# Performance work log

Measured on AMD Instinct MI355X. Metric: run time of the kernel, lower is better.

The kernel has to match this reference:

```python
import jax, jax.numpy as jnp
import numpy as np

T, B, D_IN = 1024, 64, 17
H_MAIN = 150   # per-direction hidden of main bi-GRU (hidden_dim=300)
H_HIER = 128   # per-direction hidden of hier bi-GRU (hier_hidden=256)
M = 16         # uniform measure length (eoM fires every M steps)
N_MEAS = T // M
N_PITCH, N_KS = 35, 15
PAD_P, PAD_K = 34, 14


def _gru(x, Wih, Whh, bih, bhh):
    # x: [T, N, D]; torch GRU gate order is (r, z, n)
    H = Whh.shape[1]
    gi_all = jnp.einsum('tnd,gd->tng', x, Wih) + bih  # input-side gates, precomputed

    def step(h, gi):
        gh = h @ Whh.T + bhh
        ir, iz, inn = jnp.split(gi, 3, axis=-1)
        hr, hz, hn = jnp.split(gh, 3, axis=-1)
        r = jax.nn.sigmoid(ir + hr)
        z = jax.nn.sigmoid(iz + hz)
        n = jnp.tanh(inn + r * hn)
        h_new = (1.0 - z) * n + z * h
        return h_new, h_new

    h0 = jnp.zeros((x.shape[1], H), x.dtype)
    _, ys = jax.lax.scan(step, h0, gi_all)
    return ys


def _bigru(x, pf, pb):
    yf = _gru(x, *pf)
    yb = _gru(x[::-1], *pb)[::-1]
    return jnp.concatenate([yf, yb], axis=-1)


def _ce(logits, targets, pad_idx):
    # mean cross-entropy with ignore_index=pad_idx
    logp = jax.nn.log_softmax(logits, axis=-1)
    mask = (targets != pad_idx).astype(logits.dtype)
    nll = -jnp.take_along_axis(logp, targets[:, None], axis=1)[:, 0]
    return jnp.sum(nll * mask) / jnp.maximum(jnp.sum(mask), 1.0)


def _forward(sentences, mWih_f, mWhh_f, mbih_f, mbhh_f, mWih_b, mWhh_b, mbih_b, mbhh_b,
             hWih_f, hWhh_f, hbih_f, hbhh_f, hWih_b, hWhh_b, hbih_b, hbhh_b,
             Wq, bq, Wv, bv, Wp, bp, Wk, bk, pitches, keysignatures):
    # main bi-GRU over full sequences: [T, B, 300]
    rnn_out = _bigru(sentences, (mWih_f, mWhh_f, mbih_f, mbhh_f),
                     (mWih_b, mWhh_b, mbih_b, mbhh_b))
    H2 = rnn_out.shape[-1]
    # carve uniform measures: [T,B,H2] -> [M, B*N_MEAS, H2]
    seg = rnn_out.reshape(N_MEAS, M, B, H2).transpose(1, 2, 0, 3).reshape(M, B * N_MEAS, H2)
    hier = _bigru(seg, (hWih_f, hWhh_f, hbih_f, hbhh_f),
                  (hWih_b, hWhh_b, hbih_b, hbhh_b))  # [M, B*N_MEAS, 256]
    HH = hier.shape[-1]
    # attention per measure: query = value = hier outputs [B*N_MEAS, M, 256]
    hv = hier.reshape(M, B, N_MEAS, HH).transpose(1, 2, 0, 3).reshape(B * N_MEAS, M, HH)
    q = hv @ Wq.T + bq
    v = hv @ Wv.T + bv
    attn = jax.nn.softmax(jnp.einsum('nld,nmd->nlm', q, v), axis=-1)
    ctx = jnp.einsum('nlm,nmd->nd', attn, hv).reshape(B, N_MEAS, HH)  # sum over l of attn@value
    # repeat each measure context over its M timesteps: [T, B, 256]
    ctx_t = jnp.repeat(ctx, M, axis=1).transpose(1, 0, 2)
    stacked = jnp.concatenate([rnn_out, ctx_t], axis=-1)  # [T, B, 556]
    out_pitch = stacked @ Wp.T + bp   # [T, B, 35]
    out_ks = ctx_t @ Wk.T + bk        # [T, B, 15]
    return (_ce(out_pitch.reshape(-1, N_PITCH), pitches.reshape(-1), PAD_P)
            + _ce(out_ks.reshape(-1, N_KS), keysignatures.reshape(-1), PAD_K))


def setup_inputs() -> dict:
    key = jax.random.key(0)
    ks = jax.random.split(key, 32)

    def w(i, *shape):
        return jax.random.normal(ks[i], shape, jnp.float32) * 0.05

    G_M, G_H = 3 * H_MAIN, 3 * H_HIER
    inp = {
        'sentences': jax.random.normal(ks[0], (T, B, D_IN), jnp.float32),
        'pitches': jax.random.randint(ks[1], (T, B), 0, PAD_P),
        'keysignatures': jax.random.randint(ks[2], (T, B), 0, PAD_K),
        'sentences_len': jnp.full((B,), T, dtype=jnp.int32),
        'eoM': jnp.tile(((jnp.arange(T) % M) == M - 1).astype(jnp.int32)[:, None], (1, B)),
        'mWih_f': w(3, G_M, D_IN), 'mWhh_f': w(4, G_M, H_MAIN), 'mbih_f': w(5, G_M), 'mbhh_f': w(6, G_M),
        'mWih_b': w(7, G_M, D_IN), 'mWhh_b': w(8, G_M, H_MAIN), 'mbih_b': w(9, G_M), 'mbhh_b': w(10, G_M),
        'hWih_f': w(11, G_H, 2 * H_MAIN), 'hWhh_f': w(12, G_H, H_HIER), 'hbih_f': w(13, G_H), 'hbhh_f': w(14, G_H),
        'hWih_b': w(15, G_H, 2 * H_MAIN), 'hWhh_b': w(16, G_H, H_HIER), 'hbih_b': w(17, G_H), 'hbhh_b': w(18, G_H),
        'Wq': w(19, 2 * H_HIER, 2 * H_HIER), 'bq': w(20, 2 * H_HIER),
        'Wv': w(21, 2 * H_HIER, 2 * H_HIER), 'bv': w(22, 2 * H_HIER),
        'Wp': w(23, N_PITCH, 2 * H_MAIN + 2 * H_HIER), 'bp': w(24, N_PITCH),
        'Wk': w(25, N_KS, 2 * H_HIER), 'bk': w(26, N_KS),
    }
    return inp


def reference(sentences, pitches, keysignatures, sentences_len, eoM,
              mWih_f, mWhh_f, mbih_f, mbhh_f, mWih_b, mWhh_b, mbih_b, mbhh_b,
              hWih_f, hWhh_f, hbih_f, hbhh_f, hWih_b, hWhh_b, hbih_b, hbhh_b,
              Wq, bq, Wv, bv, Wp, bp, Wk, bk):
    # sentences_len/eoM encode the (uniform) measure structure M=16, full lengths;
    # the segment layout is baked in statically, so they are structural constants here.
    return _forward(sentences, mWih_f, mWhh_f, mbih_f, mbhh_f, mWih_b, mWhh_b, mbih_b, mbhh_b,
                    hWih_f, hWhh_f, hbih_f, hbhh_f, hWih_b, hWhh_b, hbih_b, hbhh_b,
                    Wq, bq, Wv, bv, Wp, bp, Wk, bk, pitches, keysignatures)
```

## Files before the change

kernel.cpp:

```cpp
#include <hip/hip_runtime.h>
#include <cstddef>

constexpr int kT   = 1024;
constexpr int kB   = 64;
constexpr int kDIN = 17;
constexpr int kHM  = 150;
constexpr int kHH  = 128;
constexpr int kM   = 16;
constexpr int kD2  = 300;
constexpr int kNP  = 35;
constexpr int kNK  = 15;

constexpr size_t OFF_RNN16  = 0;
constexpr size_t OFF_HV16   = 10485760;
constexpr size_t OFF_PTPACK = 19988480;
constexpr size_t OFF_U      = 20021248;
constexpr size_t OFF_W      = 20021504;
constexpr size_t OFF_C0     = 20021760;
constexpr size_t OFF_ACC    = 20021776;
constexpr size_t OFF_KSLOGP = 20021792;
constexpr size_t OFF_CLOG   = 20083232;
constexpr size_t OFF_BPACK  = 20318752;
constexpr size_t OFF_BPACKL = 20490784;

typedef __bf16 bf16x8 __attribute__((ext_vector_type(8)));
typedef float f32x4 __attribute__((ext_vector_type(4)));

__device__ __forceinline__ unsigned short f2bf(float f) {
  unsigned u = __float_as_uint(f);
  u += 0x7FFFu + ((u >> 16) & 1u);
  return (unsigned short)(u >> 16);
}
__device__ __forceinline__ float bf2f(unsigned short v) {
  return __uint_as_float(((unsigned)v) << 16);
}
__device__ __forceinline__ float sigm(float x) {
  return __builtin_amdgcn_rcpf(1.f + __expf(-x));
}
__device__ __forceinline__ float tanh_fast(float x) {
  return 1.f - 2.f * __builtin_amdgcn_rcpf(__expf(2.f * x) + 1.f);
}

__global__ __launch_bounds__(640, 2) void k_mega(
    const float* __restrict__ x,
    const float* __restrict__ mWih_f, const float* __restrict__ mWhh_f,
    const float* __restrict__ mWih_b, const float* __restrict__ mWhh_b,
    const float* __restrict__ mbih_f, const float* __restrict__ mbhh_f,
    const float* __restrict__ mbih_b, const float* __restrict__ mbhh_b,
    const float* __restrict__ hWih_f, const float* __restrict__ hWhh_f,
    const float* __restrict__ hWih_b, const float* __restrict__ hWhh_b,
    const float* __restrict__ Wp,
    const float* __restrict__ Wq, const float* __restrict__ bq,
    const float* __restrict__ Wv, const float* __restrict__ bv,
    unsigned short* __restrict__ rnn16,
    unsigned short* __restrict__ bpack,
    unsigned short* __restrict__ bpackL,
    unsigned short* __restrict__ pp,
    float* __restrict__ u, float* __restrict__ w,
    float* __restrict__ c0, float* __restrict__ acc)
{
  __shared__ __align__(16) unsigned short hx[2][160];
  __shared__ __align__(16) unsigned short hist[2][16][160];
  __shared__ __align__(16) unsigned short xall[kT][32];
  const int blk = blockIdx.x;
  if (blk < 128) {
    const int d = blk & 1, b = blk >> 1;
    const int tid = threadIdx.x, wv = tid >> 6, lane = tid & 63;
    const int col = lane & 15, q8 = (lane >> 4) * 8;
    for (int i = tid; i < 2 * 160; i += 640) ((unsigned short*)hx)[i] = 0;
    for (int i = tid; i < 2 * 16 * 160; i += 640) ((unsigned short*)hist)[i] = 0;
    for (int i = tid; i < kT * 32; i += 640) {
      const int t = i >> 5, c = i & 31;
      xall[t][c] = (c < kDIN) ? f2bf(x[((size_t)t * kB + b) * kDIN + c]) : (unsigned short)0;
    }
    const float* bih = d ? mbih_b : mbih_f;
    const float* bhh = d ? mbhh_b : mbhh_f;
    const float* Wihd = d ? mWih_b : mWih_f;
    const float* Whhd = d ? mWhh_b : mWhh_f;
    const int j = wv * 16 + col;
    const bool actv = (lane < 16) && (j < kHM);
    float br = 0.f, bz = 0.f, bnx = 0.f, bnh = 0.f;
    if (actv) {
      br  = bih[j] + bhh[j];
      bz  = bih[150 + j] + bhh[150 + j];
      bnx = bih[300 + j];
      bnh = bhh[300 + j];
    }
    bf16x8 bw[3][6];
    const int gts[3] = { wv, 10 + wv, 20 + wv };
#pragma unroll
    for (int gi = 0; gi < 3; gi++) {
      const int slot = gts[gi] * 16 + col;
      const int type = slot / 160, jh = slot - type * 160;
      const int row = type * 150 + jh;
      const bool valid = (jh < 150);
#pragma unroll
      for (int kt = 0; kt < 6; kt++) {
        union { bf16x8 v; unsigned short us[8]; } tmp;
#pragma unroll
        for (int jj = 0; jj < 8; jj++) {
          float f = 0.f;
          if (valid) {
            if (kt < 5) {
              const int k = kt * 32 + (lane >> 4) * 8 + jj;
              if (k < 150) f = Whhd[row * 150 + k];
            } else {
              const int k = (lane >> 4) * 8 + jj;
              if (k < 17) f = Wihd[row * 17 + k];
            }
          }
          tmp.us[jj] = f2bf(f);
        }
        bw[gi][kt] = tmp.v;
      }
    }
    float h_old = 0.f;
    __syncthreads();

    for (int t = 0; t < kT; t++) {
      const int tx = d ? (kT - 1 - t) : t;
      const int buf = t & 1;
      bf16x8 afr[6];
#pragma unroll
      for (int kt = 0; kt < 5; kt++) afr[kt] = *(const bf16x8*)&hx[buf][kt * 32 + q8];
      afr[5] = *(const bf16x8*)&xall[tx][q8];
      f32x4 aR0 = (f32x4)(0.f), aR1 = (f32x4)(0.f);
      f32x4 aZ0 = (f32x4)(0.f), aZ1 = (f32x4)(0.f);
      f32x4 aN0 = (f32x4)(0.f), aN1 = (f32x4)(0.f);
      f32x4 aX  = (f32x4)(0.f);
#pragma unroll
      for (int kt = 0; kt < 6; kt++) {
        const bf16x8 af = afr[kt];
        if ((kt & 1) == 0) {
          aR0 = __builtin_amdgcn_mfma_f32_16x16x32_bf16(af, bw[0][kt], aR0, 0, 0, 0);
          aZ0 = __builtin_amdgcn_mfma_f32_16x16x32_bf16(af, bw[1][kt], aZ0, 0, 0, 0);
          aN0 = __builtin_amdgcn_mfma_f32_16x16x32_bf16(af, bw[2][kt], aN0, 0, 0, 0);
        } else if (kt < 5) {
          aR1 = __builtin_amdgcn_mfma_f32_16x16x32_bf16(af, bw[0][kt], aR1, 0, 0, 0);
          aZ1 = __builtin_amdgcn_mfma_f32_16x16x32_bf16(af, bw[1][kt], aZ1, 0, 0, 0);
          aN1 = __builtin_amdgcn_mfma_f32_16x16x32_bf16(af, bw[2][kt], aN1, 0, 0, 0);
        } else {
          aR1 = __builtin_amdgcn_mfma_f32_16x16x32_bf16(af, bw[0][5], aR1, 0, 0, 0);
          aZ1 = __builtin_amdgcn_mfma_f32_16x16x32_bf16(af, bw[1][5], aZ1, 0, 0, 0);
          aX  = __builtin_amdgcn_mfma_f32_16x16x32_bf16(af, bw[2][5], aX, 0, 0, 0);
        }
      }
      if (actv) {
        const float r = sigm(aR0[0] + aR1[0] + br);
        const float z = sigm(aZ0[0] + aZ1[0] + bz);
        const float n = tanh_fast(aX[0] + bnx + r * (aN0[0] + aN1[0] + bnh));
        h_old = (1.f - z) * n + z * h_old;
        const unsigned short us = f2bf(h_old);
        hx[buf ^ 1][j] = us;
        hist[(t >> 4) & 1][t & 15][j] = us;
      }
      __syncthreads();
      if ((t & 15) == 15) {
        const int hb = (t >> 4) & 1;
        const int toff = tid / 40, ch = tid - toff * 40;
        const int tg = t - 15 + toff;
        const int txg = d ? (kT - 1 - tg) : tg;
        *(ushort4*)&rnn16[((size_t)txg * kB + b) * 320 + d * 160 + ch * 4] =
            *(const ushort4*)&hist[hb][toff][ch * 4];
      }
    }
  } else if (blk < 199) {
    const int sub = threadIdx.x >> 6, lane = threadIdx.x & 63;
    int bid = (blk - 128) * 10 + sub;
    if (bid >= 702) return;
    if (bid < 672) {
      const int kt = bid % 14;
      const int nt = (bid / 14) % 24;
      const int d  = bid / (14 * 24);
      const float* Wih = d ? hWih_b : hWih_f;
      const float* Whh = d ? hWhh_b : hWhh_f;
      const int n = nt * 16 + (lane & 15);
      const int kbase = kt * 32 + (lane >> 4) * 8;
      unsigned short* dst = bpack + ((((size_t)d * 24 + nt) * 14 + kt) * 64 + lane) * 8;
#pragma unroll
      for (int jj = 0; jj < 8; jj++) {
        const int k = kbase + jj;
        float f = 0.f;
        if (kt < 10) {
          if (k < 150) f = Wih[n * 300 + k];
          else if (k >= 160 && k < 310) f = Wih[n * 300 + (k - 10)];
        } else {
          f = Whh[n * 128 + (k - 320)];
        }
        dst[jj] = f2bf(f);
      }
    } else {
      bid -= 672;
      const int kt = bid % 10, nt = bid / 10;
      const int n = nt * 16 + (lane & 15);
      const int kbase = kt * 32 + (lane >> 4) * 8;
      unsigned short* dst = bpackL + (((size_t)bid) * 64 + lane) * 8;
#pragma unroll
      for (int jj = 0; jj < 8; jj++) {
        const int k = kbase + jj;
        float f = 0.f;
        if (n < kNP) {
          if (k < 150) f = Wp[n * 556 + k];
          else if (k >= 160 && k < 310) f = Wp[n * 556 + (k - 10)];
        }
        dst[jj] = f2bf(f);
      }
    }
  } else if (blk < 212) {
    const int sub = threadIdx.x >> 6, lane = threadIdx.x & 63;
    const int bid = (blk - 199) * 10 + sub;
    if (bid >= 128) return;
    const int kt = bid & 7, nt = bid >> 3;
    const int c = nt * 16 + (lane & 15);
    const int e0 = kt * 32 + (lane >> 4) * 8;
    float av[8];
#pragma unroll
    for (int jj = 0; jj < 8; jj++) av[jj] = 0.f;
    for (int a = 0; a < 256; a++) {
      const float wq = Wq[a * 256 + c];
#pragma unroll
      for (int jj = 0; jj < 8; jj++) av[jj] += wq * Wv[a * 256 + e0 + jj];
    }
    unsigned short* dst = pp + ((size_t)bid * 64 + lane) * 8;
#pragma unroll
    for (int jj = 0; jj < 8; jj++) dst[jj] = f2bf(av[jj]);
  } else {
    const int a = threadIdx.x;
    if (a >= 256) return;
    float us = 0.f, ws = 0.f;
    for (int jj = 0; jj < 256; jj++) {
      us += Wq[jj * 256 + a] * bv[jj];
      ws += bq[jj] * Wv[jj * 256 + a];
    }
    u[a] = us; w[a] = ws;
    if (a == 0) {
      float cc = 0.f;
      for (int jj = 0; jj < 256; jj++) cc += bq[jj] * bv[jj];
      c0[0] = cc;
      acc[0] = acc[1] = acc[2] = acc[3] = 0.f;
    }
  }
}

__global__ __launch_bounds__(512, 1) void k_hier_mfma(
    const unsigned short* __restrict__ rnn16,
    const unsigned short* __restrict__ bpack,
    const float* __restrict__ bihf, const float* __restrict__ bhhf,
    const float* __restrict__ bihb, const float* __restrict__ bhhb,
    unsigned short* __restrict__ hv16)
{
  const int d = blockIdx.x & 1;
  const int bn0 = (blockIdx.x >> 1) * 16;
  const int tid = threadIdx.x;
  const int w = tid >> 6;
  const int lane = tid & 63;
  const int q = lane >> 4, col = lane & 15, q8 = q * 8;

  __shared__ __align__(16) unsigned short x_s[2][16][328];
  __shared__ __align__(16) unsigned short h_s[16][136];

  for (int i = tid; i < 16 * 136; i += 512) ((unsigned short*)h_s)[i] = 0;
  const float* bih = d ? bihb : bihf;
  const float* bhh = d ? bhhb : bhhf;
  const int j = w * 16 + col;
  const float biR  = bih[j] + bhh[j];
  const float biZ  = bih[128 + j] + bhh[128 + j];
  const float biNX = bih[256 + j];
  const float biNH = bhh[256 + j];
  float h32r[4] = {0.f, 0.f, 0.f, 0.f};

  bf16x8 bw[3][14];
  const unsigned short* bpd = bpack + (size_t)d * 24 * 14 * 64 * 8;
  const int nts[3] = { w, 8 + w, 16 + w };
#pragma unroll
  for (int gi = 0; gi < 3; gi++)
#pragma unroll
    for (int kt = 0; kt < 14; kt++)
      bw[gi][kt] = *(const bf16x8*)&bpd[(((size_t)nts[gi] * 14 + kt) * 64 + lane) * 8];

  {
    const int mx0 = d ? 15 : 0;
    for (int i = tid; i < 640; i += 512) {
      const int r = i / 40, c = i - r * 40;
      const int bn = bn0 + r, bb = bn >> 6, nn = bn & 63;
      *(uint4*)&x_s[0][r][c * 8] =
          *(const uint4*)&rnn16[((size_t)(nn * 16 + mx0) * 64 + bb) * 320 + c * 8];
    }
  }
  __syncthreads();

  for (int m = 0; m < kM; m++) {
    const int mx = d ? (15 - m) : m;
    const int buf = m & 1;
    f32x4 aR = (f32x4)(0.f), aZ = (f32x4)(0.f), aNX = (f32x4)(0.f), aNH = (f32x4)(0.f);
#pragma unroll
    for (int kt = 0; kt < 14; kt++) {
      const bf16x8 af = (kt < 10) ? *(const bf16x8*)&x_s[buf][col][kt * 32 + q8]
                                  : *(const bf16x8*)&h_s[col][(kt - 10) * 32 + q8];
      aR = __builtin_amdgcn_mfma_f32_16x16x32_bf16(af, bw[0][kt], aR, 0, 0, 0);
      aZ = __builtin_amdgcn_mfma_f32_16x16x32_bf16(af, bw[1][kt], aZ, 0, 0, 0);
      if (kt < 10) aNX = __builtin_amdgcn_mfma_f32_16x16x32_bf16(af, bw[2][kt], aNX, 0, 0, 0);
      else         aNH = __builtin_amdgcn_mfma_f32_16x16x32_bf16(af, bw[2][kt], aNH, 0, 0, 0);
    }
    __syncthreads();
#pragma unroll
    for (int i = 0; i < 4; i++) {
      const int row = q * 4 + i;
      const float rr = sigm(aR[i] + biR);
      const float zz = sigm(aZ[i] + biZ);
      const float nn2 = tanh_fast(aNX[i] + biNX + rr * (aNH[i] + biNH));
      const float hnew = (1.f - zz) * nn2 + zz * h32r[i];
      h32r[i] = hnew;
      const unsigned short us = f2bf(hnew);
      h_s[row][j] = us;
      hv16[((size_t)(bn0 + row) * kM + mx) * 256 + d * kHH + j] = us;
    }
    if (m + 1 < kM) {
      const int mxn = d ? (15 - (m + 1)) : (m + 1);
      for (int i = tid; i < 640; i += 512) {
        const int r = i / 40, c = i - r * 40;
        const int bn = bn0 + r, bb = bn >> 6, nn = bn & 63;
        *(uint4*)&x_s[buf ^ 1][r][c * 8] =
            *(const uint4*)&rnn16[((size_t)(nn * 16 + mxn) * 64 + bb) * 320 + c * 8];
      }
    }
    __syncthreads();
  }
}

__global__ __launch_bounds__(256) void k_attn_ctx(
    const unsigned short* __restrict__ hv16, const unsigned short* __restrict__ ptpack,
    const float* __restrict__ u, const float* __restrict__ w,
    const float* __restrict__ c0p,
    const float* __restrict__ Wp, const float* __restrict__ bp,
    const float* __restrict__ Wk, const float* __restrict__ bk,
    float* __restrict__ clog, float* __restrict__ kslogp) {
  const int tid = threadIdx.x;
  const int wv = tid >> 6, lane = tid & 63, col = lane & 15, q = lane >> 4, q8 = q * 8;
  __shared__ __align__(16) unsigned short hv16s[16][264];
  __shared__ __align__(16) unsigned short Ts16[16][264];
  __shared__ __align__(16) float W2[50][260];
  __shared__ __align__(16) float cs[256];
  __shared__ float pu[16][17], pw[16][17];
  __shared__ float uh[16], wh[16], SM[16];
  __shared__ float As[16][17];
  __shared__ float arr[64];
  __shared__ float bps[35], bks[15];
  const float c0 = c0p[0];
  for (int i = tid; i < 35 * 256; i += 256) { const int r = i >> 8, c = i & 255; W2[r][c] = Wp[r * 556 + 300 + c]; }
  for (int i = tid; i < 15 * 256; i += 256) { const int r = i >> 8, c = i & 255; W2[35 + r][c] = Wk[r * 256 + c]; }
  if (tid < 35) bps[tid] = bp[tid];
  else if (tid < 50) bks[tid - 35] = bk[tid - 35];
  bf16x8 bpt[4][8];
#pragma unroll
  for (int i2 = 0; i2 < 4; i2++)
#pragma unroll
    for (int kt = 0; kt < 8; kt++)
      bpt[i2][kt] = *(const bf16x8*)&ptpack[((((size_t)(wv * 4 + i2)) * 8 + kt) * 64 + lane) * 8];

  for (int ni = 0; ni < 16; ni++) {
    const int n = blockIdx.x * 16 + ni;
    {
      const unsigned short* src = hv16 + (size_t)n * 4096;
      const int row = tid >> 4, ci = (tid & 15) * 16;
#pragma unroll
      for (int k = 0; k < 16; k += 4)
        *(ushort4*)&hv16s[row][ci + k] = *(const ushort4*)&src[row * 256 + ci + k];
    }
    __syncthreads();
    {
      f32x4 acc4[4];
#pragma unroll
      for (int i2 = 0; i2 < 4; i2++) acc4[i2] = (f32x4)(0.f);
#pragma unroll
      for (int kt = 0; kt < 8; kt++) {
        const bf16x8 af = *(const bf16x8*)&hv16s[col][kt * 32 + q8];
#pragma unroll
        for (int i2 = 0; i2 < 4; i2++)
          acc4[i2] = __builtin_amdgcn_mfma_f32_16x16x32_bf16(af, bpt[i2][kt], acc4[i2], 0, 0, 0);
      }
#pragma unroll
      for (int i2 = 0; i2 < 4; i2++) {
        const int nt = wv * 4 + i2;
#pragma unroll
        for (int i = 0; i < 4; i++) Ts16[q * 4 + i][nt * 16 + col] = f2bf(acc4[i2][i]);
      }
    }
    {
      const int l = tid >> 4, s = tid & 15;
      float su = 0.f, sw = 0.f;
#pragma unroll
      for (int a0 = 0; a0 < 16; a0++) {
        const int a = s * 16 + a0;
        const float hvv = bf2f(hv16s[l][a]);
        su += hvv * u[a];
        sw += hvv * w[a];
      }
      pu[l][s] = su; pw[l][s] = sw;
    }
    __syncthreads();
    if (tid < 16) { float s2 = 0.f; for (int s = 0; s < 16; s++) s2 += pu[tid][s]; uh[tid] = s2; }
    else if (tid < 32) { float s2 = 0.f; for (int s = 0; s < 16; s++) s2 += pw[tid - 16][s]; wh[tid - 16] = s2; }
    __syncthreads();
    if (tid < 64) {
      f32x4 sa = (f32x4)(0.f);
#pragma unroll
      for (int kt = 0; kt < 8; kt++) {
        const bf16x8 af  = *(const bf16x8*)&hv16s[col][kt * 32 + q8];
        const bf16x8 bts = *(const bf16x8*)&Ts16[col][kt * 32 + q8];
        sa = __builtin_amdgcn_mfma_f32_16x16x32_bf16(af, bts, sa, 0, 0, 0);
      }
#pragma unroll
      for (int i = 0; i < 4; i++) {
        const int l = q * 4 + i;
        float sc = sa[i] + c0 + uh[l] + wh[col];
        float mxv = sc;
#pragma unroll
        for (int o = 8; o >= 1; o >>= 1) mxv = fmaxf(mxv, __shfl_xor(mxv, o, 16));
        const float e = __expf(sc - mxv);
        float se = e;
#pragma unroll
        for (int o = 8; o >= 1; o >>= 1) se += __shfl_xor(se, o, 16);
        As[l][col] = e / se;
      }
    }
    __syncthreads();
    if (tid < 16) {
      float s = 0.f;
      for (int l2 = 0; l2 < 16; l2++) s += As[l2][tid];
      SM[tid] = s;
    }
    __syncthreads();
    {
      float cv = 0.f;
#pragma unroll
      for (int m2 = 0; m2 < 16; m2++) cv += SM[m2] * bf2f(hv16s[m2][tid]);
      cs[tid] = cv;
    }
    __syncthreads();
    {
      const int o = tid >> 2, s = tid & 3;
      float v = 0.f;
      if (o < 50) {
        for (int k0 = 0; k0 < 64; k0 += 4) {
          const int k = s * 64 + k0;
          const float4 wq = *(const float4*)&W2[o][k];
          const float4 cq = *(const float4*)&cs[k];
          v += wq.x * cq.x + wq.y * cq.y + wq.z * cq.z + wq.w * cq.w;
        }
      }
      v += __shfl_xor(v, 1);
      v += __shfl_xor(v, 2);
      if (o < 50 && s == 0) arr[o] = v;
    }
    __syncthreads();
    if (tid < 35) clog[n * kNP + tid] = arr[tid] + bps[tid];
    if (tid >= 64 && tid < 80) {
      const int t2 = tid - 64;
      float kk = (t2 < 15) ? arr[35 + t2] + bks[t2] : -1e30f;
      float mxv = kk;
#pragma unroll
      for (int off = 8; off >= 1; off >>= 1) mxv = fmaxf(mxv, __shfl_xor(mxv, off, 16));
      const float e = (t2 < 15) ? __expf(kk - mxv) : 0.f;
      float se = e;
#pragma unroll
      for (int off = 8; off >= 1; off >>= 1) se += __shfl_xor(se, off, 16);
      if (t2 < 15) kslogp[n * kNK + t2] = kk - mxv - __logf(se);
    }
    __syncthreads();
  }
}

__global__ __launch_bounds__(256, 2) void k_loss_mfma(
    const unsigned short* __restrict__ rnn16,
    const unsigned short* __restrict__ bpackL,
    const float* __restrict__ clog,
    const float* __restrict__ ks_logp,
    const int* __restrict__ pitches, const int* __restrict__ kss,
    float* __restrict__ acc) {
  const int tid = threadIdx.x, w = tid >> 6, lane = tid & 63;
  const int col = lane & 15, q = lane >> 4, q8 = q * 8;
  bf16x8 bl[3][10];
#pragma unroll
  for (int nt = 0; nt < 3; nt++)
#pragma unroll
    for (int kt = 0; kt < 10; kt++)
      bl[nt][kt] = *(const bf16x8*)&bpackL[(((size_t)nt * 10 + kt) * 64 + lane) * 8];

  float sp = 0.f, cp = 0.f, sk = 0.f, ck = 0.f;
#pragma unroll
  for (int mt = 0; mt < 2; mt++) {
    const int rowbase = blockIdx.x * 128 + w * 32 + mt * 16;
    f32x4 a0 = (f32x4)(0.f), a1 = (f32x4)(0.f), a2 = (f32x4)(0.f);
#pragma unroll
    for (int kt = 0; kt < 10; kt++) {
      const bf16x8 af = *(const bf16x8*)&rnn16[(size_t)(rowbase + col) * 320 + kt * 32 + q8];
      a0 = __builtin_amdgcn_mfma_f32_16x16x32_bf16(af, bl[0][kt], a0, 0, 0, 0);
      a1 = __builtin_amdgcn_mfma_f32_16x16x32_bf16(af, bl[1][kt], a1, 0, 0, 0);
      a2 = __builtin_amdgcn_mfma_f32_16x16x32_bf16(af, bl[2][kt], a2, 0, 0, 0);
    }
#pragma unroll
    for (int i = 0; i < 4; i++) {
      const int row = rowbase + q * 4 + i;
      const int t = row >> 6, b = row & 63;
      const int bn = b * 64 + (t >> 4);
      const float lg0 = a0[i] + clog[bn * kNP + col];
      const float lg1 = a1[i] + clog[bn * kNP + 16 + col];
      const float lg2 = (col < 3) ? (a2[i] + clog[bn * kNP + 32 + col]) : -1e30f;
      float mx = fmaxf(fmaxf(lg0, lg1), lg2);
#pragma unroll
      for (int o = 8; o >= 1; o >>= 1) mx = fmaxf(mx, __shfl_xor(mx, o, 16));
      float se = __expf(lg0 - mx) + __expf(lg1 - mx) + __expf(lg2 - mx);
#pragma unroll
      for (int o = 8; o >= 1; o >>= 1) se += __shfl_xor(se, o, 16);
      const int tp = pitches[row];
      const float cand = (tp < 16) ? a0[i] : (tp < 32) ? a1[i] : a2[i];
      const float tva = __shfl(cand, (lane & 48) | (tp & 15), 64);
      if (col == 0 && tp != 34) {
        sp += (mx + __logf(se)) - (tva + clog[bn * kNP + tp]);
        cp += 1.f;
      }
      if (col == 1) {
        const int tk = kss[row];
        if (tk != 14) { sk -= ks_logp[bn * kNK + tk]; ck += 1.f; }
      }
    }
  }
#pragma unroll
  for (int o = 32; o >= 1; o >>= 1) {
    sp += __shfl_xor(sp, o, 64);
    cp += __shfl_xor(cp, o, 64);
    sk += __shfl_xor(sk, o, 64);
    ck += __shfl_xor(ck, o, 64);
  }
  if (lane == 0) {
    atomicAdd(&acc[0], sp); atomicAdd(&acc[1], cp);
    atomicAdd(&acc[2], sk); atomicAdd(&acc[3], ck);
  }
}

__global__ void k_final(const float* __restrict__ acc, float* __restrict__ out) {
  out[0] = acc[0] / fmaxf(acc[1], 1.f) + acc[2] / fmaxf(acc[3], 1.f);
}

extern "C" void kernel_launch(void* const* d_in, const int* in_sizes, int n_in,
                              void* d_out, int out_size, void* d_ws, size_t ws_size,
                              hipStream_t stream) {
  (void)in_sizes; (void)n_in; (void)out_size; (void)ws_size;
  const float* sent    = (const float*)d_in[0];
  const int*   pitches = (const int*)d_in[1];
  const int*   kss     = (const int*)d_in[2];
  const float* mWih_f  = (const float*)d_in[5];
  const float* mWhh_f  = (const float*)d_in[6];
  const float* mbih_f  = (const float*)d_in[7];
  const float* mbhh_f  = (const float*)d_in[8];
  const float* mWih_b  = (const float*)d_in[9];
  const float* mWhh_b  = (const float*)d_in[10];
  const float* mbih_b  = (const float*)d_in[11];
  const float* mbhh_b  = (const float*)d_in[12];
  const float* hWih_f  = (const float*)d_in[13];
  const float* hWhh_f  = (const float*)d_in[14];
  const float* hbih_f  = (const float*)d_in[15];
  const float* hbhh_f  = (const float*)d_in[16];
  const float* hWih_b  = (const float*)d_in[17];
  const float* hWhh_b  = (const float*)d_in[18];
  const float* hbih_b  = (const float*)d_in[19];
  const float* hbhh_b  = (const float*)d_in[20];
  const float* Wq      = (const float*)d_in[21];
  const float* bq      = (const float*)d_in[22];
  const float* Wv      = (const float*)d_in[23];
  const float* bv      = (const float*)d_in[24];
  const float* Wp      = (const float*)d_in[25];
  const float* bp      = (const float*)d_in[26];
  const float* Wk      = (const float*)d_in[27];
  const float* bk      = (const float*)d_in[28];
  float* ws  = (float*)d_ws;
  float* out = (float*)d_out;
  unsigned short* rnn16  = (unsigned short*)(ws + OFF_RNN16);
  unsigned short* hv16   = (unsigned short*)(ws + OFF_HV16);
  unsigned short* ptpack = (unsigned short*)(ws + OFF_PTPACK);
  unsigned short* bpackL = (unsigned short*)(ws + OFF_BPACKL);
  unsigned short* bpack  = (unsigned short*)(ws + OFF_BPACK);

  k_mega<<<213, 640, 0, stream>>>(sent,
                                  mWih_f, mWhh_f, mWih_b, mWhh_b,
                                  mbih_f, mbhh_f, mbih_b, mbhh_b,
                                  hWih_f, hWhh_f, hWih_b, hWhh_b, Wp,
                                  Wq, bq, Wv, bv,
                                  rnn16, bpack, bpackL, ptpack,
                                  ws + OFF_U, ws + OFF_W, ws + OFF_C0, ws + OFF_ACC);
  k_hier_mfma<<<512, 512, 0, stream>>>(rnn16, bpack,
                                       hbih_f, hbhh_f, hbih_b, hbhh_b, hv16);
  k_attn_ctx<<<256, 256, 0, stream>>>(hv16, ptpack, ws + OFF_U, ws + OFF_W,
                                      ws + OFF_C0, Wp, bp, Wk, bk,
                                      ws + OFF_CLOG, ws + OFF_KSLOGP);
  k_loss_mfma<<<512, 256, 0, stream>>>(rnn16, bpackL, ws + OFF_CLOG, ws + OFF_KSLOGP,
                                       pitches, kss, ws + OFF_ACC);
  k_final<<<1, 1, 0, stream>>>(ws + OFF_ACC, out);
}
```

Measured before the change: 1.042 ms.

## Prefetch next measure in attention kernel, double grid, fuse final reduction

The attention-context kernel now processes 8 measures per block across 512 blocks instead of 16 across 256. It register-prefetches the next measure's hier outputs while computing the current one, and caches u/w vectors in shared memory. The separate one-thread final kernel is removed: the last loss block, detected by an atomic counter, computes the output. This trims a launch and hides global load latency, at the cost of more per-block setup (W2 loads, ptpack register loads) being repeated twice as often.

```diff
diff --git a/kernel.cpp b/kernel.cpp
--- a/kernel.cpp
+++ b/kernel.cpp
@@ -237,7 +237,7 @@
       float cc = 0.f;
       for (int jj = 0; jj < 256; jj++) cc += bq[jj] * bv[jj];
       c0[0] = cc;
-      acc[0] = acc[1] = acc[2] = acc[3] = 0.f;
+      acc[0] = acc[1] = acc[2] = acc[3] = acc[4] = 0.f;
     }
   }
 }
@@ -341,6 +341,7 @@
   __shared__ __align__(16) unsigned short Ts16[16][264];
   __shared__ __align__(16) float W2[50][260];
   __shared__ __align__(16) float cs[256];
+  __shared__ __align__(16) float us[256], wss[256];
   __shared__ float pu[16][17], pw[16][17];
   __shared__ float uh[16], wh[16], SM[16];
   __shared__ float As[16][17];
@@ -349,6 +350,8 @@
   const float c0 = c0p[0];
   for (int i = tid; i < 35 * 256; i += 256) { const int r = i >> 8, c = i & 255; W2[r][c] = Wp[r * 556 + 300 + c]; }
   for (int i = tid; i < 15 * 256; i += 256) { const int r = i >> 8, c = i & 255; W2[35 + r][c] = Wk[r * 256 + c]; }
+  us[tid] = u[tid];
+  wss[tid] = w[tid];
   if (tid < 35) bps[tid] = bp[tid];
   else if (tid < 50) bks[tid - 35] = bk[tid - 35];
   bf16x8 bpt[4][8];
@@ -358,16 +361,23 @@
     for (int kt = 0; kt < 8; kt++)
       bpt[i2][kt] = *(const bf16x8*)&ptpack[((((size_t)(wv * 4 + i2)) * 8 + kt) * 64 + lane) * 8];
 
-  for (int ni = 0; ni < 16; ni++) {
-    const int n = blockIdx.x * 16 + ni;
-    {
-      const unsigned short* src = hv16 + (size_t)n * 4096;
-      const int row = tid >> 4, ci = (tid & 15) * 16;
-#pragma unroll
-      for (int k = 0; k < 16; k += 4)
-        *(ushort4*)&hv16s[row][ci + k] = *(const ushort4*)&src[row * 256 + ci + k];
-    }
-    __syncthreads();
+  const int srow = tid >> 4, sci = (tid & 15) * 16;
+  {
+    const unsigned short* src = hv16 + (size_t)(blockIdx.x * 8) * 4096;
+#pragma unroll
+    for (int k = 0; k < 16; k += 4)
+      *(ushort4*)&hv16s[srow][sci + k] = *(const ushort4*)&src[srow * 256 + sci + k];
+  }
+  __syncthreads();
+
+  for (int ni = 0; ni < 8; ni++) {
+    const int n = blockIdx.x * 8 + ni;
+    ushort4 pf[4];
+    if (ni + 1 < 8) {
+      const unsigned short* src = hv16 + (size_t)(n + 1) * 4096;
+#pragma unroll
+      for (int k2 = 0; k2 < 4; k2++) pf[k2] = *(const ushort4*)&src[srow * 256 + sci + k2 * 4];
+    }
     {
       f32x4 acc4[4];
 #pragma unroll
@@ -393,8 +403,8 @@
       for (int a0 = 0; a0 < 16; a0++) {
         const int a = s * 16 + a0;
         const float hvv = bf2f(hv16s[l][a]);
-        su += hvv * u[a];
-        sw += hvv * w[a];
+        su += hvv * us[a];
+        sw += hvv * wss[a];
       }
       pu[l][s] = su; pw[l][s] = sw;
     }
@@ -438,6 +448,10 @@
       cs[tid] = cv;
     }
     __syncthreads();
+    if (ni + 1 < 8) {
+#pragma unroll
+      for (int k2 = 0; k2 < 4; k2++) *(ushort4*)&hv16s[srow][sci + k2 * 4] = pf[k2];
+    }
     {
       const int o = tid >> 2, s = tid & 3;
       float v = 0.f;
@@ -477,7 +491,7 @@
     const float* __restrict__ clog,
     const float* __restrict__ ks_logp,
     const int* __restrict__ pitches, const int* __restrict__ kss,
-    float* __restrict__ acc) {
+    float* __restrict__ acc, float* __restrict__ out) {
   const int tid = threadIdx.x, w = tid >> 6, lane = tid & 63;
   const int col = lane & 15, q = lane >> 4, q8 = q * 8;
   bf16x8 bl[3][10];
@@ -537,10 +551,18 @@
     atomicAdd(&acc[0], sp); atomicAdd(&acc[1], cp);
     atomicAdd(&acc[2], sk); atomicAdd(&acc[3], ck);
   }
-}
-
-__global__ void k_final(const float* __restrict__ acc, float* __restrict__ out) {
-  out[0] = acc[0] / fmaxf(acc[1], 1.f) + acc[2] / fmaxf(acc[3], 1.f);
+  __syncthreads();
+  if (tid == 0) {
+    __threadfence();
+    const float done = atomicAdd(&acc[4], 1.f);
+    if (done == (float)(gridDim.x - 1)) {
+      const float a0 = atomicAdd(&acc[0], 0.f);
+      const float a1 = atomicAdd(&acc[1], 0.f);
+      const float a2 = atomicAdd(&acc[2], 0.f);
+      const float a3 = atomicAdd(&acc[3], 0.f);
+      out[0] = a0 / fmaxf(a1, 1.f) + a2 / fmaxf(a3, 1.f);
+    }
+  }
 }
 
 extern "C" void kernel_launch(void* const* d_in, const int* in_sizes, int n_in,
@@ -591,10 +613,9 @@
                                   ws + OFF_U, ws + OFF_W, ws + OFF_C0, ws + OFF_ACC);
   k_hier_mfma<<<512, 512, 0, stream>>>(rnn16, bpack,
                                        hbih_f, hbhh_f, hbih_b, hbhh_b, hv16);
-  k_attn_ctx<<<256, 256, 0, stream>>>(hv16, ptpack, ws + OFF_U, ws + OFF_W,
+  k_attn_ctx<<<512, 256, 0, stream>>>(hv16, ptpack, ws + OFF_U, ws + OFF_W,
                                       ws + OFF_C0, Wp, bp, Wk, bk,
                                       ws + OFF_CLOG, ws + OFF_KSLOGP);
   k_loss_mfma<<<512, 256, 0, stream>>>(rnn16, bpackL, ws + OFF_CLOG, ws + OFF_KSLOGP,
-                                       pitches, kss, ws + OFF_ACC);
-  k_final<<<1, 1, 0, stream>>>(ws + OFF_ACC, out);
-}
+                                       pitches, kss, ws + OFF_ACC, out);
+}
```

New measurement: 1.025 ms. Within noise of the previous version (-1.6%).
